# Optimization experiments

Hardware: AMD Instinct MI355X
Metric: run time of the kernel (lower is better)

Reference implementation:

```python
import jax, jax.numpy as jnp
import numpy as np

H = W = 32
C = 512
RED = 16


def make_gus(v=1.5):
    # gus[p=(i,k), x, y] = exp(-((x-i)^2+(y-k)^2)/(2 v^2)) / (2 pi v^2), normalized per p.
    idx = np.arange(H, dtype=np.float64)
    d2 = (idx[:, None] - idx[None, :]) ** 2          # [center, coord]
    g1 = np.exp(-d2 / (2.0 * v * v))                  # separable factor
    g = np.einsum('ix,ky->ikxy', g1, g1) / (2.0 * np.pi * v * v)
    g = g / g.sum(axis=(2, 3), keepdims=True)         # per-position normalization
    return jnp.asarray(g.reshape(H * W, H, W), dtype=jnp.float32)


def setup_inputs() -> dict:
    key = jax.random.key(0)
    ks = jax.random.split(key, 6)
    b = 16
    return {
        'x': jax.random.normal(ks[0], (b, C, H, W), dtype=jnp.float32),
        'se_w1': jax.random.normal(ks[1], (C // RED, C), dtype=jnp.float32) * 0.02,
        'se_b1': jnp.zeros((C // RED,), dtype=jnp.float32),
        'se_w2': jax.random.normal(ks[2], (C, C // RED), dtype=jnp.float32) * 0.02,
        'se_b2': jnp.zeros((C,), dtype=jnp.float32),
        'down_w': jax.random.normal(ks[3], (C, 2 * C), dtype=jnp.float32) * 0.02,
        'gus': make_gus(1.5),
    }


def _patches3(img, h, w):
    # img: [b, c, h+2, w+2] -> [b, c, h, w, 9] (3x3 neighborhoods, row-major dy*3+dx)
    ps = [img[:, :, dy:dy + h, dx:dx + w] for dy in range(3) for dx in range(3)]
    return jnp.stack(ps, axis=-1)


def reference(x, se_w1, se_b1, se_w2, se_b2, down_w, gus):
    b, c, h, w = x.shape
    # --- SELayer ---
    s = x.mean(axis=(2, 3))                                   # [b, c]
    y = jax.nn.relu(s @ se_w1.T + se_b1)                       # [b, c/16]
    y = jax.nn.sigmoid(y @ se_w2.T + se_b2)                    # [b, c]
    out32 = x * y[:, :, None, None]
    # --- gaussian-weighted global pooling per output position ---
    # g[b, p, ch] = sum_{y,x} gus[p,y,x] * out32[b,ch,y,x]; then torch's view(c,h,w)
    gus_out = jnp.einsum('pyx,bcyx->bpc', gus, out32).reshape(b, c, h, w)
    # --- patch self-attention ---
    sig = jax.nn.sigmoid(out32)
    sigp = _patches3(jnp.pad(sig, ((0, 0), (0, 0), (1, 1), (1, 1))), h, w)    # [b,c,h,w,9]
    ffp = _patches3(jnp.pad(out32, ((0, 0), (0, 0), (1, 1), (1, 1))), h, w)   # [b,c,h,w,9]
    logits = jnp.einsum('bcyx,bcyxk->byxk', sig, sigp) / c     # mean over channels
    attn = jax.nn.softmax(logits, axis=-1)                     # softmax over 3x3 patch
    g2 = jnp.einsum('byxk,bcyxk->byxc', attn, ffp)             # [b,h,w,c] = [b, p, c]
    out_csa = g2.reshape(b, c, h, w)                           # torch view(c,h,w) of [hw,c]
    # --- down: 1x1 conv (no bias) + InstanceNorm2d + LeakyReLU(0.2) ---
    cat = jnp.concatenate([gus_out, out_csa], axis=1)          # [b, 2c, h, w]
    z = jnp.einsum('oi,biyx->boyx', down_w, cat)
    mu = z.mean(axis=(2, 3), keepdims=True)
    var = z.var(axis=(2, 3), keepdims=True)
    zn = (z - mu) * jax.lax.rsqrt(var + 1e-5)
    return jnp.where(zn >= 0, zn, 0.2 * zn)
```

## Files before the change

kernel.cpp:

```cpp
#include <hip/hip_runtime.h>
#include <stdint.h>

#define NB 16
#define NC 512
#define NS 1024
#define NR 32

typedef unsigned short u16;
typedef unsigned int u32;

typedef __attribute__((ext_vector_type(8))) short short8;
typedef __attribute__((ext_vector_type(4))) float f32x4;

__device__ __forceinline__ float bf2f(u16 u) {
    union { u32 i; float f; } c; c.i = ((u32)u) << 16; return c.f;
}
__device__ __forceinline__ u16 f2bf(float f) {
    union { float f; u32 i; } c; c.f = f;
    u32 r = (c.i + 0x7FFFu + ((c.i >> 16) & 1u)) >> 16;
    return (u16)r;
}
__device__ __forceinline__ float sigm(float x) {
    return 1.0f / (1.0f + __expf(-x));
}

__global__ void k_mean_cvt(const float* __restrict__ x, float* __restrict__ sm,
                           const float* __restrict__ dw, u16* __restrict__ dwb) {
    const int t = threadIdx.x;
    if (blockIdx.x < NB * NC) {
        const int row = blockIdx.x;
        const float4* xr = (const float4*)(x + (long)row * NS);
        float4 v = xr[t];
        float p = v.x + v.y + v.z + v.w;
        for (int off = 32; off; off >>= 1) p += __shfl_down(p, off);
        __shared__ __align__(16) float red[4];
        if ((t & 63) == 0) red[t >> 6] = p;
        __syncthreads();
        if (t == 0) sm[row] = (red[0] + red[1] + red[2] + red[3]) * (1.0f / 1024.0f);
    } else {
        const int i = (blockIdx.x - NB * NC) * 256 + t;
        dwb[i] = f2bf(dw[i]);
    }
}

__global__ __launch_bounds__(256)
void k_gusT(const float* __restrict__ g, u16* __restrict__ gt) {
    const int p0 = (blockIdx.x & 15) * 64;
    const int k0 = (blockIdx.x >> 4) * 64;
    const int t = threadIdx.x;
    __shared__ float tile[64][65];
#pragma unroll
    for (int it = 0; it < 4; ++it) {
        int c = it * 256 + t;
        int row = c >> 4;
        int f4 = c & 15;
        float4 v = *(const float4*)&g[(long)(p0 + row) * 1024 + k0 + f4 * 4];
        tile[row][f4 * 4 + 0] = v.x; tile[row][f4 * 4 + 1] = v.y;
        tile[row][f4 * 4 + 2] = v.z; tile[row][f4 * 4 + 3] = v.w;
    }
    __syncthreads();
    const int q = t >> 7, k_loc = t & 63, h = (t >> 6) & 1;
    short8 v0, v1;
#pragma unroll
    for (int jj = 0; jj < 8; ++jj) {
        v0[jj] = (short)f2bf(tile[2 * (h * 16 + jj) + q][k_loc]);
        v1[jj] = (short)f2bf(tile[2 * (h * 16 + 8 + jj) + q][k_loc]);
    }
    long ob = (long)q * 524288 + (long)(k0 + k_loc) * 512 + (p0 >> 1) + h * 16;
    *(short8*)&gt[ob] = v0;
    *(short8*)&gt[ob + 8] = v1;
}

__global__ void k_se(const float* __restrict__ sm, const float* __restrict__ w1,
                     const float* __restrict__ b1, const float* __restrict__ w2,
                     const float* __restrict__ b2, float* __restrict__ y) {
    const int b = blockIdx.x;
    __shared__ __align__(16) float s_s[NC];
    __shared__ __align__(16) float s_y1[NR];
    const int t = threadIdx.x;
    s_s[t] = sm[b * NC + t];
    s_s[t + 256] = sm[b * NC + t + 256];
    __syncthreads();
    {
        const int r = t >> 3, sub = t & 7;
        const float4* wr = (const float4*)(w1 + r * NC + sub * 64);
        const float4* sv = (const float4*)(s_s + sub * 64);
        float acc = 0.f;
#pragma unroll
        for (int i = 0; i < 16; ++i) {
            float4 wv = wr[i];
            float4 s4 = sv[i];
            acc += wv.x * s4.x + wv.y * s4.y + wv.z * s4.z + wv.w * s4.w;
        }
        acc += __shfl_down(acc, 4);
        acc += __shfl_down(acc, 2);
        acc += __shfl_down(acc, 1);
        if (sub == 0) s_y1[r] = fmaxf(acc + b1[r], 0.0f);
    }
    __syncthreads();
    for (int i = 0; i < 2; ++i) {
        int c = t + i * 256;
        float acc = b2[c];
#pragma unroll
        for (int r = 0; r < NR; ++r) acc += s_y1[r] * w2[c * NR + r];
        y[b * NC + c] = 1.0f / (1.0f + expf(-acc));
    }
}

__global__ void k_scale(const float* __restrict__ x, const float* __restrict__ y,
                        u16* __restrict__ o32, u16* __restrict__ o32t) {
    const int b = blockIdx.z;
    const int c0 = blockIdx.y * 32;
    const int s0 = blockIdx.x * 32;
    const int tx = threadIdx.x & 31, ty = threadIdx.x >> 5;
    __shared__ float tile[32][33];
    const float* xb = x + (long)b * NC * NS;
#pragma unroll
    for (int it = 0; it < 4; ++it) {
        int c = c0 + ty + it * 8;
        float v = xb[(long)c * NS + s0 + tx] * y[b * NC + c];
        tile[ty + it * 8][tx] = v;
        o32[((long)b * NC + c) * NS + s0 + tx] = f2bf(v);
    }
    __syncthreads();
#pragma unroll
    for (int it = 0; it < 4; ++it) {
        int sr = ty + it * 8;
        float tv = tile[tx][sr];
        long idx = ((long)b * NS + (s0 + sr)) * NC + c0 + tx;
        o32t[idx] = f2bf(tv);
    }
}

__global__ __launch_bounds__(256)
void gemm_bt(const u16* __restrict__ A, const u16* __restrict__ Bt, u16* __restrict__ Co,
             int K, long batA, long batB, long batC, int ldc, int lda, int ldb) {
    const int b = blockIdx.z;
    const u16* Ab = A + (long)b * batA;
    const u16* Bb = Bt + (long)b * batB;
    u16* Cb = Co + (long)b * batC;
    const int m0 = blockIdx.y * 128;
    const int n0 = blockIdx.x * 128;
    __shared__ __align__(16) u16 As[128 * 128];
    __shared__ __align__(16) u16 Bs[128 * 128];
    const int tid = threadIdx.x;
    const int lane = tid & 63, wave = tid >> 6;
    const int wm = (wave >> 1) * 64, wn = (wave & 1) * 64;
    f32x4 acc[4][4];
#pragma unroll
    for (int i = 0; i < 4; ++i)
#pragma unroll
        for (int j = 0; j < 4; ++j) acc[i][j] = (f32x4){0.f, 0.f, 0.f, 0.f};

    int srow[8], sg8[8];
#pragma unroll
    for (int r = 0; r < 8; ++r) {
        int c = r * 256 + tid;
        srow[r] = c >> 4;
        sg8[r] = ((c & 15) ^ (srow[r] & 15)) * 8;
    }

    for (int k0 = 0; k0 < K; k0 += 128) {
#pragma unroll
        for (int r = 0; r < 8; ++r) {
            const int c = r * 256 + tid;
            const u16* ga = Ab + (long)(m0 + srow[r]) * lda + (k0 + sg8[r]);
            __builtin_amdgcn_global_load_lds(
                (const __attribute__((address_space(1))) u32*)ga,
                (__attribute__((address_space(3))) u32*)&As[c * 8], 16, 0, 0);
            const u16* gb = Bb + (long)(n0 + srow[r]) * ldb + (k0 + sg8[r]);
            __builtin_amdgcn_global_load_lds(
                (const __attribute__((address_space(1))) u32*)gb,
                (__attribute__((address_space(3))) u32*)&Bs[c * 8], 16, 0, 0);
        }
        __syncthreads();
#pragma unroll
        for (int kk = 0; kk < 128; kk += 32) {
            const int gq = (kk >> 3) + (lane >> 4);
            const int slot = gq ^ (lane & 15);
            short8 af[4], bfr[4];
#pragma unroll
            for (int i = 0; i < 4; ++i)
                af[i] = *(const short8*)&As[(wm + i * 16 + (lane & 15)) * 128 + slot * 8];
#pragma unroll
            for (int j = 0; j < 4; ++j)
                bfr[j] = *(const short8*)&Bs[(wn + j * 16 + (lane & 15)) * 128 + slot * 8];
#pragma unroll
            for (int i = 0; i < 4; ++i)
#pragma unroll
                for (int j = 0; j < 4; ++j)
                    acc[i][j] = __builtin_amdgcn_mfma_f32_16x16x32_bf16(af[i], bfr[j], acc[i][j], 0, 0, 0);
        }
        __syncthreads();
    }
    const int col = lane & 15, rq = (lane >> 4) * 4;
#pragma unroll
    for (int i = 0; i < 4; ++i)
#pragma unroll
        for (int j = 0; j < 4; ++j)
#pragma unroll
            for (int r = 0; r < 4; ++r) {
                int row = m0 + wm + i * 16 + rq + r;
                int ncol = n0 + wn + j * 16 + col;
                Cb[(long)row * ldc + ncol] = f2bf(acc[i][j][r]);
            }
}

__global__ __launch_bounds__(256)
void k_zgemm(const u16* __restrict__ Em, const u16* __restrict__ dwb,
             const u16* __restrict__ o32, const u16* __restrict__ gsep,
             u16* __restrict__ Z) {
    const int b = blockIdx.z;
    const int band = blockIdx.y & 1;
    const int m0 = (blockIdx.y >> 1) * 128;
    const int n0 = blockIdx.x * 128;
    __shared__ __align__(16) u16 As[128 * 128];
    __shared__ __align__(16) u16 Bs[128 * 128];
    const int tid = threadIdx.x;
    const int lane = tid & 63, wave = tid >> 6;
    const int wm = (wave >> 1) * 64, wn = (wave & 1) * 64;
    f32x4 acc[4][4];
#pragma unroll
    for (int i = 0; i < 4; ++i)
#pragma unroll
        for (int j = 0; j < 4; ++j) acc[i][j] = (f32x4){0.f, 0.f, 0.f, 0.f};

    int srow[8], sg8[8];
#pragma unroll
    for (int r = 0; r < 8; ++r) {
        int c = r * 256 + tid;
        srow[r] = c >> 4;
        sg8[r] = ((c & 15) ^ (srow[r] & 15)) * 8;
    }
    const u16* A0 = Em + (long)band * 524288;
    const u16* B0 = o32 + (long)b * 524288;
    const u16* B1 = gsep + (long)b * 524288 + (long)band * 262144;

    for (int k0 = 0; k0 < 1536; k0 += 128) {
#pragma unroll
        for (int r = 0; r < 8; ++r) {
            const int c = r * 256 + tid;
            const u16* ga;
            const u16* gb;
            if (k0 < 1024) {
                ga = A0 + (long)(m0 + srow[r]) * 1024 + (k0 + sg8[r]);
                gb = B0 + (long)(n0 + srow[r]) * 1024 + (k0 + sg8[r]);
            } else {
                ga = dwb + (long)(m0 + srow[r]) * 1024 + 512 + (k0 - 1024) + sg8[r];
                gb = B1 + (long)(n0 + srow[r]) * 512 + (k0 - 1024) + sg8[r];
            }
            __builtin_amdgcn_global_load_lds(
                (const __attribute__((address_space(1))) u32*)ga,
                (__attribute__((address_space(3))) u32*)&As[c * 8], 16, 0, 0);
            __builtin_amdgcn_global_load_lds(
                (const __attribute__((address_space(1))) u32*)gb,
                (__attribute__((address_space(3))) u32*)&Bs[c * 8], 16, 0, 0);
        }
        __syncthreads();
#pragma unroll
        for (int kk = 0; kk < 128; kk += 32) {
            const int gq = (kk >> 3) + (lane >> 4);
            const int slot = gq ^ (lane & 15);
            short8 af[4], bfr[4];
#pragma unroll
            for (int i = 0; i < 4; ++i)
                af[i] = *(const short8*)&As[(wm + i * 16 + (lane & 15)) * 128 + slot * 8];
#pragma unroll
            for (int j = 0; j < 4; ++j)
                bfr[j] = *(const short8*)&Bs[(wn + j * 16 + (lane & 15)) * 128 + slot * 8];
#pragma unroll
            for (int i = 0; i < 4; ++i)
#pragma unroll
                for (int j = 0; j < 4; ++j)
                    acc[i][j] = __builtin_amdgcn_mfma_f32_16x16x32_bf16(af[i], bfr[j], acc[i][j], 0, 0, 0);
        }
        __syncthreads();
    }
    const int col = lane & 15, rq = (lane >> 4) * 4;
#pragma unroll
    for (int i = 0; i < 4; ++i)
#pragma unroll
        for (int j = 0; j < 4; ++j)
#pragma unroll
            for (int r = 0; r < 4; ++r) {
                int row = m0 + wm + i * 16 + rq + r;
                int ncol = n0 + wn + j * 16 + col;
                Z[((long)b * 512 + row) * 1024 + band * 512 + ncol] = f2bf(acc[i][j][r]);
            }
}

__global__ __launch_bounds__(256)
void k_attn(const u16* __restrict__ o32t, u16* __restrict__ g2) {
    const int wave = threadIdx.x >> 6, lane = threadIdx.x & 63;
    const int tid = threadIdx.x;
    const int bx = blockIdx.x;
    const int b = blockIdx.y;
    const int y0 = bx >> 3;
    const int xbase = (bx & 7) * 4;
    const long base = (long)b * NS * NC;
    __shared__ __align__(16) u16 smem[2 * 18 * NC];

#pragma unroll
    for (int r = 0; r < 5; ++r) {
        int idx = r * 256 + tid;
        if (idx < 18 * 64) {
            int pair = idx >> 6;
            int ch0 = (idx & 63) * 8;
            int yy = y0 + pair / 6 - 1;
            int xx = xbase + pair % 6 - 1;
            short8 v = (short8){0, 0, 0, 0, 0, 0, 0, 0};
            short8 sv = (short8){0, 0, 0, 0, 0, 0, 0, 0};
            if (yy >= 0 && yy < 32 && xx >= 0 && xx < 32) {
                v = *(const short8*)&o32t[base + (long)(yy * 32 + xx) * NC + ch0];
#pragma unroll
                for (int j = 0; j < 8; ++j) sv[j] = (short)f2bf(sigm(bf2f((u16)v[j])));
            }
            *(short8*)&smem[(18 + pair) * NC + ch0] = v;
            *(short8*)&smem[pair * NC + ch0] = sv;
        }
    }
    __syncthreads();

    const int coff = lane * 8;
    short8 csv = *(const short8*)&smem[(6 + wave + 1) * NC + coff];
    float sc[8];
#pragma unroll
    for (int j = 0; j < 8; ++j) sc[j] = bf2f((u16)csv[j]);

    float part[9];
#pragma unroll
    for (int k = 0; k < 9; ++k) {
        int pair = (k / 3) * 6 + wave + k % 3;
        short8 sv = *(const short8*)&smem[pair * NC + coff];
        float p = 0.f;
#pragma unroll
        for (int j = 0; j < 8; ++j) p += sc[j] * bf2f((u16)sv[j]);
        part[k] = p;
    }
#pragma unroll
    for (int k = 0; k < 9; ++k)
        for (int off = 32; off; off >>= 1) part[k] += __shfl_down(part[k], off);

    if (lane == 0) {
        float mx = -1e30f;
#pragma unroll
        for (int k = 0; k < 9; ++k) { part[k] *= (1.0f / 512.0f); mx = fmaxf(mx, part[k]); }
        float sum = 0.f;
#pragma unroll
        for (int k = 0; k < 9; ++k) { part[k] = __expf(part[k] - mx); sum += part[k]; }
        float inv = 1.0f / sum;
#pragma unroll
        for (int k = 0; k < 9; ++k) part[k] *= inv;
    }
    float g[8] = {0.f, 0.f, 0.f, 0.f, 0.f, 0.f, 0.f, 0.f};
#pragma unroll
    for (int k = 0; k < 9; ++k) {
        float a = __shfl(part[k], 0);
        int pair = (k / 3) * 6 + wave + k % 3;
        short8 rv = *(const short8*)&smem[(18 + pair) * NC + coff];
#pragma unroll
        for (int j = 0; j < 8; ++j) g[j] += a * bf2f((u16)rv[j]);
    }
    short8 ov;
#pragma unroll
    for (int j = 0; j < 8; ++j) ov[j] = (short)f2bf(g[j]);
    const int s = y0 * 32 + xbase + wave;
    *(short8*)&g2[base + (long)s * NC + coff] = ov;
}

__global__ __launch_bounds__(256)
void k_tr2(const u16* __restrict__ g2, u16* __restrict__ gs) {
    long idx = (long)blockIdx.x * 256 + threadIdx.x;
    int c = (int)(idx & 511);
    int rest = (int)(idx >> 9);
    int jc = rest & 31;
    int q = (rest >> 5) & 1;
    int b = rest >> 6;
    const u16* src = g2 + (long)b * 524288;
    short8 v0, v1;
#pragma unroll
    for (int jj = 0; jj < 8; ++jj) {
        v0[jj] = (short)src[(long)(2 * (jc * 16 + jj) + q) * 512 + c];
        v1[jj] = (short)src[(long)(2 * (jc * 16 + 8 + jj) + q) * 512 + c];
    }
    long ob = (long)b * 524288 + (long)q * 262144 + (long)c * 512 + jc * 16;
    *(short8*)&gs[ob] = v0;
    *(short8*)&gs[ob + 8] = v1;
}

__global__ void k_norm(const u16* __restrict__ z, float* __restrict__ out) {
    const int row = blockIdx.x;
    const int t = threadIdx.x;
    uint2 u = ((const uint2*)(z + (long)row * NS))[t];
    float v0 = bf2f((u16)(u.x & 0xffffu)), v1 = bf2f((u16)(u.x >> 16));
    float v2 = bf2f((u16)(u.y & 0xffffu)), v3 = bf2f((u16)(u.y >> 16));
    float sm = v0 + v1 + v2 + v3;
    float sq = v0 * v0 + v1 * v1 + v2 * v2 + v3 * v3;
    for (int off = 32; off; off >>= 1) { sm += __shfl_down(sm, off); sq += __shfl_down(sq, off); }
    __shared__ __align__(16) float rs[4], rq2[4];
    if ((t & 63) == 0) { rs[t >> 6] = sm; rq2[t >> 6] = sq; }
    __syncthreads();
    float tot = rs[0] + rs[1] + rs[2] + rs[3];
    float totq = rq2[0] + rq2[1] + rq2[2] + rq2[3];
    float mu = tot * (1.0f / 1024.0f);
    float var = totq * (1.0f / 1024.0f) - mu * mu;
    float sc = rsqrtf(var + 1e-5f);
    float4 o;
    float a;
    a = (v0 - mu) * sc; o.x = (a >= 0.f) ? a : 0.2f * a;
    a = (v1 - mu) * sc; o.y = (a >= 0.f) ? a : 0.2f * a;
    a = (v2 - mu) * sc; o.z = (a >= 0.f) ? a : 0.2f * a;
    a = (v3 - mu) * sc; o.w = (a >= 0.f) ? a : 0.2f * a;
    ((float4*)(out + (long)row * NS))[t] = o;
}

extern "C" void kernel_launch(void* const* d_in, const int* in_sizes, int n_in,
                              void* d_out, int out_size, void* d_ws, size_t ws_size,
                              hipStream_t stream) {
    const float* x   = (const float*)d_in[0];
    const float* w1  = (const float*)d_in[1];
    const float* b1  = (const float*)d_in[2];
    const float* w2  = (const float*)d_in[3];
    const float* b2  = (const float*)d_in[4];
    const float* dw  = (const float*)d_in[5];
    const float* gus = (const float*)d_in[6];
    float* out = (float*)d_out;
    char* ws = (char*)d_ws;

    float* sm_buf = (float*)(ws + 0);
    float* y_buf  = (float*)(ws + 32768);
    u16* dwbf     = (u16*)(ws + 65536);
    u16* gusTb    = (u16*)(ws + 1114112);
    u16* Ebuf     = (u16*)(ws + 3211264);
    u16* o32      = (u16*)(ws + 5308416);
    u16* o32t     = (u16*)(ws + 22085632);
    u16* g2b      = (u16*)(ws + 38862848);
    u16* g2sep    = (u16*)(ws + 22085632);
    u16* Z        = (u16*)(ws + 38862848);

    k_mean_cvt<<<dim3(NB * NC + 2048), dim3(256), 0, stream>>>(x, sm_buf, dw, dwbf);
    k_gusT<<<dim3(256), dim3(256), 0, stream>>>(gus, gusTb);
    k_se<<<dim3(NB), dim3(256), 0, stream>>>(sm_buf, w1, b1, w2, b2, y_buf);
    gemm_bt<<<dim3(8, 4, 2), dim3(256), 0, stream>>>(
        dwbf, gusTb, Ebuf, 512, 0L, 524288L, 524288L, 1024, 1024, 512);
    k_scale<<<dim3(32, 16, NB), dim3(256), 0, stream>>>(x, y_buf, o32, o32t);
    k_attn<<<dim3(256, NB), dim3(256), 0, stream>>>(o32t, g2b);
    k_tr2<<<dim3(2048), dim3(256), 0, stream>>>(g2b, g2sep);
    k_zgemm<<<dim3(4, 8, NB), dim3(256), 0, stream>>>(Ebuf, dwbf, o32, g2sep, Z);
    k_norm<<<dim3(NB * NC), dim3(256), 0, stream>>>(Z, out);
}
```

Before: 200.2 us.

## Merge small launches, tile k_tr2 through LDS, split zgemm K loop

Folds k_gusT into the mean/convert kernel and runs the SE MLP in the same launch as the weight-by-gaussian GEMM, cutting the launch count from nine to seven. k_tr2 now moves each 64x64 tile through swizzled shared memory so that global reads and writes are vector-wide and coalesced, where before it made strided scalar loads. k_zgemm's K loop is split into two loops so the per-iteration branch on which source to load disappears. The larger shared-memory footprint of k_pre may lower occupancy for the mean blocks.

```diff
diff --git a/kernel.cpp b/kernel.cpp
--- a/kernel.cpp
+++ b/kernel.cpp
@@ -24,8 +24,15 @@
     return 1.0f / (1.0f + __expf(-x));
 }
 
-__global__ void k_mean_cvt(const float* __restrict__ x, float* __restrict__ sm,
-                           const float* __restrict__ dw, u16* __restrict__ dwb) {
+#define GLD16(gp, lp)                                                      \
+    __builtin_amdgcn_global_load_lds(                                      \
+        (const __attribute__((address_space(1))) u32*)(gp),                \
+        (__attribute__((address_space(3))) u32*)(lp), 16, 0, 0)
+
+__global__ void k_pre(const float* __restrict__ x, float* __restrict__ sm,
+                      const float* __restrict__ dw, u16* __restrict__ dwb,
+                      const float* __restrict__ g, u16* __restrict__ gt) {
+    __shared__ __align__(16) float shb[64 * 65];
     const int t = threadIdx.x;
     if (blockIdx.x < NB * NC) {
         const int row = blockIdx.x;
@@ -33,77 +40,143 @@
         float4 v = xr[t];
         float p = v.x + v.y + v.z + v.w;
         for (int off = 32; off; off >>= 1) p += __shfl_down(p, off);
-        __shared__ __align__(16) float red[4];
-        if ((t & 63) == 0) red[t >> 6] = p;
-        __syncthreads();
-        if (t == 0) sm[row] = (red[0] + red[1] + red[2] + red[3]) * (1.0f / 1024.0f);
-    } else {
+        if ((t & 63) == 0) shb[t >> 6] = p;
+        __syncthreads();
+        if (t == 0) sm[row] = (shb[0] + shb[1] + shb[2] + shb[3]) * (1.0f / 1024.0f);
+    } else if (blockIdx.x < NB * NC + 2048) {
         const int i = (blockIdx.x - NB * NC) * 256 + t;
         dwb[i] = f2bf(dw[i]);
-    }
-}
+    } else {
+        const int gbx = blockIdx.x - (NB * NC + 2048);
+        const int p0 = (gbx & 15) * 64;
+        const int k0 = (gbx >> 4) * 64;
+        float (*tile)[65] = (float(*)[65])shb;
+#pragma unroll
+        for (int it = 0; it < 4; ++it) {
+            int c = it * 256 + t;
+            int row = c >> 4;
+            int f4 = c & 15;
+            float4 v = *(const float4*)&g[(long)(p0 + row) * 1024 + k0 + f4 * 4];
+            tile[row][f4 * 4 + 0] = v.x; tile[row][f4 * 4 + 1] = v.y;
+            tile[row][f4 * 4 + 2] = v.z; tile[row][f4 * 4 + 3] = v.w;
+        }
+        __syncthreads();
+        const int q = t >> 7, k_loc = t & 63, h = (t >> 6) & 1;
+        short8 v0, v1;
+#pragma unroll
+        for (int jj = 0; jj < 8; ++jj) {
+            v0[jj] = (short)f2bf(tile[2 * (h * 16 + jj) + q][k_loc]);
+            v1[jj] = (short)f2bf(tile[2 * (h * 16 + 8 + jj) + q][k_loc]);
+        }
+        long ob = (long)q * 524288 + (long)(k0 + k_loc) * 512 + (p0 >> 1) + h * 16;
+        *(short8*)&gt[ob] = v0;
+        *(short8*)&gt[ob + 8] = v1;
+    }
+}
+
+#define MFMA_TILE_STEP(As, Bs)                                                      \
+    {                                                                               \
+        _Pragma("unroll")                                                           \
+        for (int kk = 0; kk < 128; kk += 32) {                                      \
+            const int gq = (kk >> 3) + (lane >> 4);                                 \
+            const int slot = gq ^ (lane & 15);                                      \
+            short8 af[4], bfr[4];                                                   \
+            _Pragma("unroll")                                                       \
+            for (int i = 0; i < 4; ++i)                                             \
+                af[i] = *(const short8*)&As[(wm + i * 16 + (lane & 15)) * 128 + slot * 8]; \
+            _Pragma("unroll")                                                       \
+            for (int j = 0; j < 4; ++j)                                             \
+                bfr[j] = *(const short8*)&Bs[(wn + j * 16 + (lane & 15)) * 128 + slot * 8]; \
+            _Pragma("unroll")                                                       \
+            for (int i = 0; i < 4; ++i)                                             \
+                _Pragma("unroll")                                                   \
+                for (int j = 0; j < 4; ++j)                                         \
+                    acc[i][j] = __builtin_amdgcn_mfma_f32_16x16x32_bf16(af[i], bfr[j], acc[i][j], 0, 0, 0); \
+        }                                                                           \
+    }
 
 __global__ __launch_bounds__(256)
-void k_gusT(const float* __restrict__ g, u16* __restrict__ gt) {
-    const int p0 = (blockIdx.x & 15) * 64;
-    const int k0 = (blockIdx.x >> 4) * 64;
-    const int t = threadIdx.x;
-    __shared__ float tile[64][65];
-#pragma unroll
-    for (int it = 0; it < 4; ++it) {
-        int c = it * 256 + t;
-        int row = c >> 4;
-        int f4 = c & 15;
-        float4 v = *(const float4*)&g[(long)(p0 + row) * 1024 + k0 + f4 * 4];
-        tile[row][f4 * 4 + 0] = v.x; tile[row][f4 * 4 + 1] = v.y;
-        tile[row][f4 * 4 + 2] = v.z; tile[row][f4 * 4 + 3] = v.w;
-    }
-    __syncthreads();
-    const int q = t >> 7, k_loc = t & 63, h = (t >> 6) & 1;
-    short8 v0, v1;
-#pragma unroll
-    for (int jj = 0; jj < 8; ++jj) {
-        v0[jj] = (short)f2bf(tile[2 * (h * 16 + jj) + q][k_loc]);
-        v1[jj] = (short)f2bf(tile[2 * (h * 16 + 8 + jj) + q][k_loc]);
-    }
-    long ob = (long)q * 524288 + (long)(k0 + k_loc) * 512 + (p0 >> 1) + h * 16;
-    *(short8*)&gt[ob] = v0;
-    *(short8*)&gt[ob + 8] = v1;
-}
-
-__global__ void k_se(const float* __restrict__ sm, const float* __restrict__ w1,
-                     const float* __restrict__ b1, const float* __restrict__ w2,
-                     const float* __restrict__ b2, float* __restrict__ y) {
-    const int b = blockIdx.x;
-    __shared__ __align__(16) float s_s[NC];
-    __shared__ __align__(16) float s_y1[NR];
-    const int t = threadIdx.x;
-    s_s[t] = sm[b * NC + t];
-    s_s[t + 256] = sm[b * NC + t + 256];
-    __syncthreads();
-    {
-        const int r = t >> 3, sub = t & 7;
-        const float4* wr = (const float4*)(w1 + r * NC + sub * 64);
-        const float4* sv = (const float4*)(s_s + sub * 64);
-        float acc = 0.f;
-#pragma unroll
-        for (int i = 0; i < 16; ++i) {
-            float4 wv = wr[i];
-            float4 s4 = sv[i];
-            acc += wv.x * s4.x + wv.y * s4.y + wv.z * s4.z + wv.w * s4.w;
-        }
-        acc += __shfl_down(acc, 4);
-        acc += __shfl_down(acc, 2);
-        acc += __shfl_down(acc, 1);
-        if (sub == 0) s_y1[r] = fmaxf(acc + b1[r], 0.0f);
-    }
-    __syncthreads();
-    for (int i = 0; i < 2; ++i) {
-        int c = t + i * 256;
-        float acc = b2[c];
-#pragma unroll
-        for (int r = 0; r < NR; ++r) acc += s_y1[r] * w2[c * NR + r];
-        y[b * NC + c] = 1.0f / (1.0f + expf(-acc));
+void k_we(const u16* __restrict__ dwb, const u16* __restrict__ gt,
+          u16* __restrict__ Eb, const float* __restrict__ sm,
+          const float* __restrict__ w1, const float* __restrict__ b1,
+          const float* __restrict__ w2, const float* __restrict__ b2,
+          float* __restrict__ y) {
+    __shared__ __align__(16) u16 As[128 * 128];
+    __shared__ __align__(16) u16 Bs[128 * 128];
+    const int bx = blockIdx.x;
+    const int tid = threadIdx.x;
+    if (bx < 64) {
+        const int q = bx >> 5, rem = bx & 31;
+        const int m0 = (rem >> 3) * 128, n0 = (rem & 7) * 128;
+        const u16* Bb = gt + (long)q * 524288;
+        const int lane = tid & 63, wave = tid >> 6;
+        const int wm = (wave >> 1) * 64, wn = (wave & 1) * 64;
+        f32x4 acc[4][4];
+#pragma unroll
+        for (int i = 0; i < 4; ++i)
+#pragma unroll
+            for (int j = 0; j < 4; ++j) acc[i][j] = (f32x4){0.f, 0.f, 0.f, 0.f};
+        int srow[8], sg8[8];
+#pragma unroll
+        for (int r = 0; r < 8; ++r) {
+            int c = r * 256 + tid;
+            srow[r] = c >> 4;
+            sg8[r] = ((c & 15) ^ (srow[r] & 15)) * 8;
+        }
+        for (int k0 = 0; k0 < 512; k0 += 128) {
+#pragma unroll
+            for (int r = 0; r < 8; ++r) {
+                const int c = r * 256 + tid;
+                GLD16(dwb + (long)(m0 + srow[r]) * 1024 + (k0 + sg8[r]), &As[c * 8]);
+                GLD16(Bb + (long)(n0 + srow[r]) * 512 + (k0 + sg8[r]), &Bs[c * 8]);
+            }
+            __syncthreads();
+            MFMA_TILE_STEP(As, Bs);
+            __syncthreads();
+        }
+        const int col = lane & 15, rq = (lane >> 4) * 4;
+#pragma unroll
+        for (int i = 0; i < 4; ++i)
+#pragma unroll
+            for (int j = 0; j < 4; ++j)
+#pragma unroll
+                for (int r = 0; r < 4; ++r) {
+                    int row = m0 + wm + i * 16 + rq + r;
+                    int ncol = n0 + wn + j * 16 + col;
+                    Eb[(long)q * 524288 + (long)row * 1024 + ncol] = f2bf(acc[i][j][r]);
+                }
+    } else {
+        const int b = bx - 64;
+        float* s_s = (float*)As;
+        float* s_y1 = (float*)Bs;
+        const int t = tid;
+        s_s[t] = sm[b * NC + t];
+        s_s[t + 256] = sm[b * NC + t + 256];
+        __syncthreads();
+        {
+            const int r = t >> 3, sub = t & 7;
+            const float4* wr = (const float4*)(w1 + r * NC + sub * 64);
+            const float4* sv = (const float4*)(s_s + sub * 64);
+            float acc = 0.f;
+#pragma unroll
+            for (int i = 0; i < 16; ++i) {
+                float4 wv = wr[i];
+                float4 s4 = sv[i];
+                acc += wv.x * s4.x + wv.y * s4.y + wv.z * s4.z + wv.w * s4.w;
+            }
+            acc += __shfl_down(acc, 4);
+            acc += __shfl_down(acc, 2);
+            acc += __shfl_down(acc, 1);
+            if (sub == 0) s_y1[r] = fmaxf(acc + b1[r], 0.0f);
+        }
+        __syncthreads();
+        for (int i = 0; i < 2; ++i) {
+            int c = t + i * 256;
+            float acc = b2[c];
+#pragma unroll
+            for (int r = 0; r < NR; ++r) acc += s_y1[r] * w2[c * NR + r];
+            y[b * NC + c] = 1.0f / (1.0f + expf(-acc));
+        }
     }
 }
 
@@ -133,77 +206,117 @@
 }
 
 __global__ __launch_bounds__(256)
-void gemm_bt(const u16* __restrict__ A, const u16* __restrict__ Bt, u16* __restrict__ Co,
-             int K, long batA, long batB, long batC, int ldc, int lda, int ldb) {
-    const int b = blockIdx.z;
-    const u16* Ab = A + (long)b * batA;
-    const u16* Bb = Bt + (long)b * batB;
-    u16* Cb = Co + (long)b * batC;
-    const int m0 = blockIdx.y * 128;
-    const int n0 = blockIdx.x * 128;
-    __shared__ __align__(16) u16 As[128 * 128];
-    __shared__ __align__(16) u16 Bs[128 * 128];
+void k_attn(const u16* __restrict__ o32t, u16* __restrict__ g2) {
+    const int wave = threadIdx.x >> 6, lane = threadIdx.x & 63;
     const int tid = threadIdx.x;
-    const int lane = tid & 63, wave = tid >> 6;
-    const int wm = (wave >> 1) * 64, wn = (wave & 1) * 64;
-    f32x4 acc[4][4];
-#pragma unroll
-    for (int i = 0; i < 4; ++i)
-#pragma unroll
-        for (int j = 0; j < 4; ++j) acc[i][j] = (f32x4){0.f, 0.f, 0.f, 0.f};
-
-    int srow[8], sg8[8];
-#pragma unroll
-    for (int r = 0; r < 8; ++r) {
-        int c = r * 256 + tid;
-        srow[r] = c >> 4;
-        sg8[r] = ((c & 15) ^ (srow[r] & 15)) * 8;
-    }
-
-    for (int k0 = 0; k0 < K; k0 += 128) {
-#pragma unroll
-        for (int r = 0; r < 8; ++r) {
-            const int c = r * 256 + tid;
-            const u16* ga = Ab + (long)(m0 + srow[r]) * lda + (k0 + sg8[r]);
-            __builtin_amdgcn_global_load_lds(
-                (const __attribute__((address_space(1))) u32*)ga,
-                (__attribute__((address_space(3))) u32*)&As[c * 8], 16, 0, 0);
-            const u16* gb = Bb + (long)(n0 + srow[r]) * ldb + (k0 + sg8[r]);
-            __builtin_amdgcn_global_load_lds(
-                (const __attribute__((address_space(1))) u32*)gb,
-                (__attribute__((address_space(3))) u32*)&Bs[c * 8], 16, 0, 0);
-        }
-        __syncthreads();
-#pragma unroll
-        for (int kk = 0; kk < 128; kk += 32) {
-            const int gq = (kk >> 3) + (lane >> 4);
-            const int slot = gq ^ (lane & 15);
-            short8 af[4], bfr[4];
-#pragma unroll
-            for (int i = 0; i < 4; ++i)
-                af[i] = *(const short8*)&As[(wm + i * 16 + (lane & 15)) * 128 + slot * 8];
-#pragma unroll
-            for (int j = 0; j < 4; ++j)
-                bfr[j] = *(const short8*)&Bs[(wn + j * 16 + (lane & 15)) * 128 + slot * 8];
-#pragma unroll
-            for (int i = 0; i < 4; ++i)
-#pragma unroll
-                for (int j = 0; j < 4; ++j)
-                    acc[i][j] = __builtin_amdgcn_mfma_f32_16x16x32_bf16(af[i], bfr[j], acc[i][j], 0, 0, 0);
-        }
-        __syncthreads();
-    }
-    const int col = lane & 15, rq = (lane >> 4) * 4;
-#pragma unroll
-    for (int i = 0; i < 4; ++i)
-#pragma unroll
-        for (int j = 0; j < 4; ++j)
-#pragma unroll
-            for (int r = 0; r < 4; ++r) {
-                int row = m0 + wm + i * 16 + rq + r;
-                int ncol = n0 + wn + j * 16 + col;
-                Cb[(long)row * ldc + ncol] = f2bf(acc[i][j][r]);
+    const int bx = blockIdx.x;
+    const int b = blockIdx.y;
+    const int y0 = bx >> 3;
+    const int xbase = (bx & 7) * 4;
+    const long base = (long)b * NS * NC;
+    __shared__ __align__(16) u16 smem[2 * 18 * NC];
+
+#pragma unroll
+    for (int r = 0; r < 5; ++r) {
+        int idx = r * 256 + tid;
+        if (idx < 18 * 64) {
+            int pair = idx >> 6;
+            int ch0 = (idx & 63) * 8;
+            int yy = y0 + pair / 6 - 1;
+            int xx = xbase + pair % 6 - 1;
+            short8 v = (short8){0, 0, 0, 0, 0, 0, 0, 0};
+            short8 sv = (short8){0, 0, 0, 0, 0, 0, 0, 0};
+            if (yy >= 0 && yy < 32 && xx >= 0 && xx < 32) {
+                v = *(const short8*)&o32t[base + (long)(yy * 32 + xx) * NC + ch0];
+#pragma unroll
+                for (int j = 0; j < 8; ++j) sv[j] = (short)f2bf(sigm(bf2f((u16)v[j])));
             }
+            *(short8*)&smem[(18 + pair) * NC + ch0] = v;
+            *(short8*)&smem[pair * NC + ch0] = sv;
+        }
+    }
+    __syncthreads();
+
+    const int coff = lane * 8;
+    short8 csv = *(const short8*)&smem[(6 + wave + 1) * NC + coff];
+    float sc[8];
+#pragma unroll
+    for (int j = 0; j < 8; ++j) sc[j] = bf2f((u16)csv[j]);
+
+    float part[9];
+#pragma unroll
+    for (int k = 0; k < 9; ++k) {
+        int pair = (k / 3) * 6 + wave + k % 3;
+        short8 sv = *(const short8*)&smem[pair * NC + coff];
+        float p = 0.f;
+#pragma unroll
+        for (int j = 0; j < 8; ++j) p += sc[j] * bf2f((u16)sv[j]);
+        part[k] = p;
+    }
+#pragma unroll
+    for (int k = 0; k < 9; ++k)
+        for (int off = 32; off; off >>= 1) part[k] += __shfl_down(part[k], off);
+
+    if (lane == 0) {
+        float mx = -1e30f;
+#pragma unroll
+        for (int k = 0; k < 9; ++k) { part[k] *= (1.0f / 512.0f); mx = fmaxf(mx, part[k]); }
+        float sum = 0.f;
+#pragma unroll
+        for (int k = 0; k < 9; ++k) { part[k] = __expf(part[k] - mx); sum += part[k]; }
+        float inv = 1.0f / sum;
+#pragma unroll
+        for (int k = 0; k < 9; ++k) part[k] *= inv;
+    }
+    float g[8] = {0.f, 0.f, 0.f, 0.f, 0.f, 0.f, 0.f, 0.f};
+#pragma unroll
+    for (int k = 0; k < 9; ++k) {
+        float a = __shfl(part[k], 0);
+        int pair = (k / 3) * 6 + wave + k % 3;
+        short8 rv = *(const short8*)&smem[(18 + pair) * NC + coff];
+#pragma unroll
+        for (int j = 0; j < 8; ++j) g[j] += a * bf2f((u16)rv[j]);
+    }
+    short8 ov;
+#pragma unroll
+    for (int j = 0; j < 8; ++j) ov[j] = (short)f2bf(g[j]);
+    const int s = y0 * 32 + xbase + wave;
+    *(short8*)&g2[base + (long)s * NC + coff] = ov;
+}
+
+__global__ __launch_bounds__(256)
+void k_tr2(const u16* __restrict__ g2, u16* __restrict__ gs) {
+    const int b = blockIdx.y;
+    const int c0 = (blockIdx.x & 7) * 64;
+    const int j0 = ((blockIdx.x >> 3) & 7) * 64;
+    const int q = blockIdx.x >> 6;
+    const int t = threadIdx.x;
+    __shared__ __align__(16) u16 tile[64 * 64];
+    const u16* src = g2 + (long)b * 524288 + (long)(2 * j0 + q) * 512 + c0;
+#pragma unroll
+    for (int it = 0; it < 2; ++it) {
+        int c = it * 256 + t;
+        int jl = c >> 3, sg = c & 7;
+        short8 v = *(const short8*)&src[(long)jl * 1024 + sg * 8];
+        int slot = sg ^ ((jl >> 3) & 7);
+        *(short8*)&tile[jl * 64 + slot * 8] = v;
+    }
+    __syncthreads();
+#pragma unroll
+    for (int it = 0; it < 2; ++it) {
+        int c = it * 256 + t;
+        int cl = c >> 3, jg = c & 7;
+        const int gcs = cl >> 3, co = cl & 7;
+        short8 v;
+#pragma unroll
+        for (int jj = 0; jj < 8; ++jj) {
+            int j = jg * 8 + jj;
+            int slot = gcs ^ jg;
+            v[jj] = (short)tile[j * 64 + slot * 8 + co];
+        }
+        *(short8*)&gs[(long)b * 524288 + (long)q * 262144 +
+                      (long)(c0 + cl) * 512 + j0 + jg * 8] = v;
+    }
 }
 
 __global__ __launch_bounds__(256)
@@ -234,46 +347,29 @@
     }
     const u16* A0 = Em + (long)band * 524288;
     const u16* B0 = o32 + (long)b * 524288;
+    const u16* A1 = dwb + 512;
     const u16* B1 = gsep + (long)b * 524288 + (long)band * 262144;
 
-    for (int k0 = 0; k0 < 1536; k0 += 128) {
+    for (int k0 = 0; k0 < 1024; k0 += 128) {
 #pragma unroll
         for (int r = 0; r < 8; ++r) {
             const int c = r * 256 + tid;
-            const u16* ga;
-            const u16* gb;
-            if (k0 < 1024) {
-                ga = A0 + (long)(m0 + srow[r]) * 1024 + (k0 + sg8[r]);
-                gb = B0 + (long)(n0 + srow[r]) * 1024 + (k0 + sg8[r]);
-            } else {
-                ga = dwb + (long)(m0 + srow[r]) * 1024 + 512 + (k0 - 1024) + sg8[r];
-                gb = B1 + (long)(n0 + srow[r]) * 512 + (k0 - 1024) + sg8[r];
-            }
-            __builtin_amdgcn_global_load_lds(
-                (const __attribute__((address_space(1))) u32*)ga,
-                (__attribute__((address_space(3))) u32*)&As[c * 8], 16, 0, 0);
-            __builtin_amdgcn_global_load_lds(
-                (const __attribute__((address_space(1))) u32*)gb,
-                (__attribute__((address_space(3))) u32*)&Bs[c * 8], 16, 0, 0);
-        }
-        __syncthreads();
-#pragma unroll
-        for (int kk = 0; kk < 128; kk += 32) {
-            const int gq = (kk >> 3) + (lane >> 4);
-            const int slot = gq ^ (lane & 15);
-            short8 af[4], bfr[4];
-#pragma unroll
-            for (int i = 0; i < 4; ++i)
-                af[i] = *(const short8*)&As[(wm + i * 16 + (lane & 15)) * 128 + slot * 8];
-#pragma unroll
-            for (int j = 0; j < 4; ++j)
-                bfr[j] = *(const short8*)&Bs[(wn + j * 16 + (lane & 15)) * 128 + slot * 8];
-#pragma unroll
-            for (int i = 0; i < 4; ++i)
-#pragma unroll
-                for (int j = 0; j < 4; ++j)
-                    acc[i][j] = __builtin_amdgcn_mfma_f32_16x16x32_bf16(af[i], bfr[j], acc[i][j], 0, 0, 0);
-        }
+            GLD16(A0 + (long)(m0 + srow[r]) * 1024 + (k0 + sg8[r]), &As[c * 8]);
+            GLD16(B0 + (long)(n0 + srow[r]) * 1024 + (k0 + sg8[r]), &Bs[c * 8]);
+        }
+        __syncthreads();
+        MFMA_TILE_STEP(As, Bs);
+        __syncthreads();
+    }
+    for (int k0 = 0; k0 < 512; k0 += 128) {
+#pragma unroll
+        for (int r = 0; r < 8; ++r) {
+            const int c = r * 256 + tid;
+            GLD16(A1 + (long)(m0 + srow[r]) * 1024 + (k0 + sg8[r]), &As[c * 8]);
+            GLD16(B1 + (long)(n0 + srow[r]) * 512 + (k0 + sg8[r]), &Bs[c * 8]);
+        }
+        __syncthreads();
+        MFMA_TILE_STEP(As, Bs);
         __syncthreads();
     }
     const int col = lane & 15, rq = (lane >> 4) * 4;
@@ -287,105 +383,6 @@
                 int ncol = n0 + wn + j * 16 + col;
                 Z[((long)b * 512 + row) * 1024 + band * 512 + ncol] = f2bf(acc[i][j][r]);
             }
-}
-
-__global__ __launch_bounds__(256)
-void k_attn(const u16* __restrict__ o32t, u16* __restrict__ g2) {
-    const int wave = threadIdx.x >> 6, lane = threadIdx.x & 63;
-    const int tid = threadIdx.x;
-    const int bx = blockIdx.x;
-    const int b = blockIdx.y;
-    const int y0 = bx >> 3;
-    const int xbase = (bx & 7) * 4;
-    const long base = (long)b * NS * NC;
-    __shared__ __align__(16) u16 smem[2 * 18 * NC];
-
-#pragma unroll
-    for (int r = 0; r < 5; ++r) {
-        int idx = r * 256 + tid;
-        if (idx < 18 * 64) {
-            int pair = idx >> 6;
-            int ch0 = (idx & 63) * 8;
-            int yy = y0 + pair / 6 - 1;
-            int xx = xbase + pair % 6 - 1;
-            short8 v = (short8){0, 0, 0, 0, 0, 0, 0, 0};
-            short8 sv = (short8){0, 0, 0, 0, 0, 0, 0, 0};
-            if (yy >= 0 && yy < 32 && xx >= 0 && xx < 32) {
-                v = *(const short8*)&o32t[base + (long)(yy * 32 + xx) * NC + ch0];
-#pragma unroll
-                for (int j = 0; j < 8; ++j) sv[j] = (short)f2bf(sigm(bf2f((u16)v[j])));
-            }
-            *(short8*)&smem[(18 + pair) * NC + ch0] = v;
-            *(short8*)&smem[pair * NC + ch0] = sv;
-        }
-    }
-    __syncthreads();
-
-    const int coff = lane * 8;
-    short8 csv = *(const short8*)&smem[(6 + wave + 1) * NC + coff];
-    float sc[8];
-#pragma unroll
-    for (int j = 0; j < 8; ++j) sc[j] = bf2f((u16)csv[j]);
-
-    float part[9];
-#pragma unroll
-    for (int k = 0; k < 9; ++k) {
-        int pair = (k / 3) * 6 + wave + k % 3;
-        short8 sv = *(const short8*)&smem[pair * NC + coff];
-        float p = 0.f;
-#pragma unroll
-        for (int j = 0; j < 8; ++j) p += sc[j] * bf2f((u16)sv[j]);
-        part[k] = p;
-    }
-#pragma unroll
-    for (int k = 0; k < 9; ++k)
-        for (int off = 32; off; off >>= 1) part[k] += __shfl_down(part[k], off);
-
-    if (lane == 0) {
-        float mx = -1e30f;
-#pragma unroll
-        for (int k = 0; k < 9; ++k) { part[k] *= (1.0f / 512.0f); mx = fmaxf(mx, part[k]); }
-        float sum = 0.f;
-#pragma unroll
-        for (int k = 0; k < 9; ++k) { part[k] = __expf(part[k] - mx); sum += part[k]; }
-        float inv = 1.0f / sum;
-#pragma unroll
-        for (int k = 0; k < 9; ++k) part[k] *= inv;
-    }
-    float g[8] = {0.f, 0.f, 0.f, 0.f, 0.f, 0.f, 0.f, 0.f};
-#pragma unroll
-    for (int k = 0; k < 9; ++k) {
-        float a = __shfl(part[k], 0);
-        int pair = (k / 3) * 6 + wave + k % 3;
-        short8 rv = *(const short8*)&smem[(18 + pair) * NC + coff];
-#pragma unroll
-        for (int j = 0; j < 8; ++j) g[j] += a * bf2f((u16)rv[j]);
-    }
-    short8 ov;
-#pragma unroll
-    for (int j = 0; j < 8; ++j) ov[j] = (short)f2bf(g[j]);
-    const int s = y0 * 32 + xbase + wave;
-    *(short8*)&g2[base + (long)s * NC + coff] = ov;
-}
-
-__global__ __launch_bounds__(256)
-void k_tr2(const u16* __restrict__ g2, u16* __restrict__ gs) {
-    long idx = (long)blockIdx.x * 256 + threadIdx.x;
-    int c = (int)(idx & 511);
-    int rest = (int)(idx >> 9);
-    int jc = rest & 31;
-    int q = (rest >> 5) & 1;
-    int b = rest >> 6;
-    const u16* src = g2 + (long)b * 524288;
-    short8 v0, v1;
-#pragma unroll
-    for (int jj = 0; jj < 8; ++jj) {
-        v0[jj] = (short)src[(long)(2 * (jc * 16 + jj) + q) * 512 + c];
-        v1[jj] = (short)src[(long)(2 * (jc * 16 + 8 + jj) + q) * 512 + c];
-    }
-    long ob = (long)b * 524288 + (long)q * 262144 + (long)c * 512 + jc * 16;
-    *(short8*)&gs[ob] = v0;
-    *(short8*)&gs[ob + 8] = v1;
 }
 
 __global__ void k_norm(const u16* __restrict__ z, float* __restrict__ out) {
@@ -438,14 +435,13 @@
     u16* g2sep    = (u16*)(ws + 22085632);
     u16* Z        = (u16*)(ws + 38862848);
 
-    k_mean_cvt<<<dim3(NB * NC + 2048), dim3(256), 0, stream>>>(x, sm_buf, dw, dwbf);
-    k_gusT<<<dim3(256), dim3(256), 0, stream>>>(gus, gusTb);
-    k_se<<<dim3(NB), dim3(256), 0, stream>>>(sm_buf, w1, b1, w2, b2, y_buf);
-    gemm_bt<<<dim3(8, 4, 2), dim3(256), 0, stream>>>(
-        dwbf, gusTb, Ebuf, 512, 0L, 524288L, 524288L, 1024, 1024, 512);
+    k_pre<<<dim3(NB * NC + 2048 + 256), dim3(256), 0, stream>>>(
+        x, sm_buf, dw, dwbf, gus, gusTb);
+    k_we<<<dim3(80), dim3(256), 0, stream>>>(
+        dwbf, gusTb, Ebuf, sm_buf, w1, b1, w2, b2, y_buf);
     k_scale<<<dim3(32, 16, NB), dim3(256), 0, stream>>>(x, y_buf, o32, o32t);
     k_attn<<<dim3(256, NB), dim3(256), 0, stream>>>(o32t, g2b);
-    k_tr2<<<dim3(2048), dim3(256), 0, stream>>>(g2b, g2sep);
+    k_tr2<<<dim3(128, NB), dim3(256), 0, stream>>>(g2b, g2sep);
     k_zgemm<<<dim3(4, 8, NB), dim3(256), 0, stream>>>(Ebuf, dwbf, o32, g2sep, Z);
     k_norm<<<dim3(NB * NC), dim3(256), 0, stream>>>(Z, out);
 }
```

New measurement: 193.4 us. 3.4% less time.
